# Kernel tuning notes

Hardware: AMD Instinct MI355X
Metric: run time of the kernel (lower is better)

The kernel has to match this reference:

```python
import jax, jax.numpy as jnp
import numpy as np

B, T, C = 2, 2048, 2048
NUM_HEADS, NUM_KV_HEADS, HEAD_DIM = 16, 4, 128
ROPE_THETA = 10000.0
SOFTCAP = 50.0


def sine_table(features, length, min_timescale=1.0, max_timescale=10000.0):
    fraction = jnp.arange(0, features, 2, dtype=jnp.float32) / features
    timescale = min_timescale * (max_timescale / min_timescale) ** fraction
    sinusoid = jnp.arange(length, dtype=jnp.float32)[:, None] / timescale[None, :]
    sinusoid = jnp.concatenate([sinusoid, sinusoid], axis=-1)
    return jnp.sin(sinusoid), jnp.cos(sinusoid)


def rotate_half(x):
    x1, x2 = jnp.split(x, 2, axis=-1)
    return jnp.concatenate([-x2, x1], axis=-1)


def setup_inputs() -> dict:
    key = jax.random.key(0)
    k1, k2, k3, k4, k5 = jax.random.split(key, 5)
    x = jax.random.normal(k1, (B, T, C), dtype=jnp.float32)
    mask = jnp.tril(jnp.ones((T, T), dtype=bool))[None, None]  # causal [1,1,T,T]
    mask = jnp.broadcast_to(mask, (B, 1, T, T))
    std = 0.02
    q_kernel = std * jax.random.normal(k2, (C, NUM_HEADS * HEAD_DIM), dtype=jnp.float32)
    k_kernel = std * jax.random.normal(k3, (C, NUM_KV_HEADS * HEAD_DIM), dtype=jnp.float32)
    v_kernel = std * jax.random.normal(k4, (C, NUM_KV_HEADS * HEAD_DIM), dtype=jnp.float32)
    out_kernel = std * jax.random.normal(k5, (NUM_HEADS * HEAD_DIM, C), dtype=jnp.float32)
    return {"x": x, "mask": mask, "q_kernel": q_kernel, "k_kernel": k_kernel,
            "v_kernel": v_kernel, "out_kernel": out_kernel}


def reference(x, mask, q_kernel, k_kernel, v_kernel, out_kernel):
    _, t, c = x.shape
    r = NUM_HEADS // NUM_KV_HEADS  # GQA group size
    qp = q_kernel.reshape(c, r, NUM_KV_HEADS, HEAD_DIM)
    kp = k_kernel.reshape(c, NUM_KV_HEADS, HEAD_DIM)
    vp = v_kernel.reshape(c, NUM_KV_HEADS, HEAD_DIM)
    op = out_kernel.reshape(r, NUM_KV_HEADS, HEAD_DIM, c)
    q = jnp.einsum('bsm,mrhk->brhsk', x, qp)   # [B,r,h,T,hd]
    k = jnp.einsum('bdm,mhk->bhdk', x, kp)     # [B,h,T,hd]
    v = jnp.einsum('bdm,mhv->bhdv', x, vp)     # [B,h,T,hd]
    sin, cos = sine_table(HEAD_DIM, t, max_timescale=ROPE_THETA)  # [T,hd]
    q = q * cos + rotate_half(q) * sin  # broadcast over leading dims (time at -2)
    k = k * cos + rotate_half(k) * sin
    scale = jax.lax.rsqrt(jnp.array(HEAD_DIM, dtype=x.dtype))
    qk = jnp.einsum('brhsk,bhdk->brhsd', q, k) * scale  # [B,r,h,T,T]
    qk = jnp.tanh(qk / SOFTCAP) * SOFTCAP  # logit softcap
    m = jnp.expand_dims(mask, axis=1)  # [B,1,1,T,T]
    qk = jax.nn.softmax(qk.astype(jnp.float32), where=m).astype(x.dtype)
    qkv = jnp.einsum('brhsd,bhdv->brhsv', qk, v)
    out = jnp.einsum('brhsv,rhvm->bsm', qkv, op)
    return out
```

## Files before the change

### kernel.cpp

```cpp
#include <hip/hip_runtime.h>
#include <hip/hip_bf16.h>

typedef __hip_bfloat16 bf16;
typedef __attribute__((ext_vector_type(8))) short bf16x8;
typedef __attribute__((ext_vector_type(4))) short bf16x4;
typedef __attribute__((ext_vector_type(4))) float f32x4;

#define BATCH 2
#define SEQ 2048
#define CDIM 2048
#define NH 16
#define NKV 4
#define HD 128
#define NQKV 3072

__device__ __forceinline__ float tof(float x)  { return x; }
__device__ __forceinline__ float tof(bf16 x)   { return __bfloat162float(x); }
__device__ __forceinline__ void  stf(float* p, float v) { *p = v; }
__device__ __forceinline__ void  stf(bf16* p,  float v) { *p = __float2bfloat16(v); }

__device__ __forceinline__ void gl_lds16(const bf16* g, bf16* l) {
    typedef const __attribute__((address_space(1))) unsigned int* gp_t;
    typedef __attribute__((address_space(3))) unsigned int* lp_t;
    __builtin_amdgcn_global_load_lds((gp_t)g, (lp_t)l, 16, 0, 0);
}

__device__ __forceinline__ f32x4 mfma16x16x16_bf16(bf16x4 a, bf16x4 b, f32x4 c) {
#if __has_builtin(__builtin_amdgcn_mfma_f32_16x16x16bf16_1k)
    return __builtin_amdgcn_mfma_f32_16x16x16bf16_1k(a, b, c, 0, 0, 0);
#else
    asm volatile("v_mfma_f32_16x16x16_bf16 %0, %1, %2, %0"
                 : "+v"(c) : "v"(a), "v"(b));
    return c;
#endif
}

__device__ __forceinline__ float fast_exp2(float x) {
#if __has_builtin(__builtin_amdgcn_exp2f)
    return __builtin_amdgcn_exp2f(x);
#else
    return exp2f(x);
#endif
}

__global__ __launch_bounds__(256) void f2b_kernel(const float* __restrict__ in,
                                                  bf16* __restrict__ out, int n4)
{
    int i = blockIdx.x * 256 + threadIdx.x;
    if (i >= n4) return;
    float4 v = *(const float4*)&in[(size_t)i * 4];
    bf16 o[4] = {__float2bfloat16(v.x), __float2bfloat16(v.y),
                 __float2bfloat16(v.z), __float2bfloat16(v.w)};
    *(ushort4*)&out[(size_t)i * 4] = *(ushort4*)o;
}

__global__ __launch_bounds__(256) void transpose_f2b_kernel(
    const float* __restrict__ in, bf16* __restrict__ out, int R, int Cn)
{
    __shared__ float tile[64][65];
    const int r0 = blockIdx.y * 64, c0 = blockIdx.x * 64;
    for (int f = threadIdx.x; f < 4096; f += 256) {
        int r = f >> 6, c = f & 63;
        tile[r][c] = in[(size_t)(r0 + r) * Cn + c0 + c];
    }
    __syncthreads();
    for (int f = threadIdx.x; f < 4096; f += 256) {
        int r = f >> 6, c = f & 63;
        out[(size_t)(c0 + r) * R + r0 + c] = __float2bfloat16(tile[c][r]);
    }
}

__global__ __launch_bounds__(256) void vtrans_kernel(
    const bf16* __restrict__ in, bf16* __restrict__ out)
{
    __shared__ bf16 tile[64][65];
    const int b = blockIdx.z;
    const int t0 = blockIdx.y * 64, c0 = blockIdx.x * 64;
    for (int f = threadIdx.x; f < 4096; f += 256) {
        int r = f >> 6, c = f & 63;
        tile[r][c] = in[(size_t)(b * SEQ + t0 + r) * (NKV * HD) + c0 + c];
    }
    __syncthreads();
    for (int f = threadIdx.x; f < 4096; f += 256) {
        int r = f >> 6, c = f & 63;
        out[(size_t)(b * NKV * HD + c0 + r) * SEQ + t0 + c] = tile[c][r];
    }
}

__global__ __launch_bounds__(256) void gemm_qkv_kernel(
    const bf16* __restrict__ A, const bf16* __restrict__ Bt,
    bf16* __restrict__ Qr, bf16* __restrict__ Kr, bf16* __restrict__ Vr,
    int M, int K)
{
    __shared__ __align__(16) bf16 As[128 * 32];
    __shared__ __align__(16) bf16 Bs[128 * 32];

    const int tid = threadIdx.x;
    const int lane = tid & 63;
    const int wave = tid >> 6;
    const int m0 = blockIdx.y * 128;
    const int n0 = blockIdx.x * 128;
    const int wm = (wave >> 1) * 64;
    const int wn = (wave & 1) * 64;
    const int quad = lane >> 4;
    const int l16 = lane & 15;

    const int srow = tid >> 2;
    const int scol = (tid & 3) * 8;
    const bf16* Ag0 = A  + (size_t)(m0 + srow) * K + scol;
    const bf16* Ag1 = A  + (size_t)(m0 + srow + 64) * K + scol;
    const bf16* Bg0 = Bt + (size_t)(n0 + srow) * K + scol;
    const bf16* Bg1 = Bt + (size_t)(n0 + srow + 64) * K + scol;

    f32x4 acc[4][4];
#pragma unroll
    for (int mi = 0; mi < 4; ++mi)
#pragma unroll
        for (int ni = 0; ni < 4; ++ni)
            acc[mi][ni] = (f32x4){0.f, 0.f, 0.f, 0.f};

    for (int kt = 0; kt < K; kt += 32) {
        __syncthreads();
        gl_lds16(Ag0 + kt, &As[tid * 8]);
        gl_lds16(Ag1 + kt, &As[2048 + tid * 8]);
        gl_lds16(Bg0 + kt, &Bs[tid * 8]);
        gl_lds16(Bg1 + kt, &Bs[2048 + tid * 8]);
        __syncthreads();

        bf16x8 a[4], b[4];
#pragma unroll
        for (int mi = 0; mi < 4; ++mi)
            a[mi] = *(const bf16x8*)&As[(wm + mi * 16 + l16) * 32 + quad * 8];
#pragma unroll
        for (int ni = 0; ni < 4; ++ni)
            b[ni] = *(const bf16x8*)&Bs[(wn + ni * 16 + l16) * 32 + quad * 8];
#pragma unroll
        for (int mi = 0; mi < 4; ++mi)
#pragma unroll
            for (int ni = 0; ni < 4; ++ni)
                acc[mi][ni] = __builtin_amdgcn_mfma_f32_16x16x32_bf16(
                    a[mi], b[ni], acc[mi][ni], 0, 0, 0);
    }

    bf16* Cp; int Nst, cbase;
    if (n0 < 2048)      { Cp = Qr; Nst = 2048; cbase = n0; }
    else if (n0 < 2560) { Cp = Kr; Nst = 512;  cbase = n0 - 2048; }
    else                { Cp = Vr; Nst = 512;  cbase = n0 - 2560; }

#pragma unroll
    for (int mi = 0; mi < 4; ++mi)
#pragma unroll
        for (int ni = 0; ni < 4; ++ni) {
            int col = cbase + wn + ni * 16 + l16;
#pragma unroll
            for (int r = 0; r < 4; ++r) {
                int row = m0 + wm + mi * 16 + quad * 4 + r;
                Cp[(size_t)row * Nst + col] = __float2bfloat16(acc[mi][ni][r]);
            }
        }
}

template <typename TC>
__global__ __launch_bounds__(256) void gemm_mfma_bt(
    const bf16* __restrict__ A, const bf16* __restrict__ Bt, TC* __restrict__ C,
    int M, int N, int K)
{
    __shared__ __align__(16) bf16 As[128 * 32];
    __shared__ __align__(16) bf16 Bs[128 * 32];

    const int tid = threadIdx.x;
    const int lane = tid & 63;
    const int wave = tid >> 6;
    const int m0 = blockIdx.y * 128;
    const int n0 = blockIdx.x * 128;
    const int wm = (wave >> 1) * 64;
    const int wn = (wave & 1) * 64;
    const int quad = lane >> 4;
    const int l16 = lane & 15;

    const int srow = tid >> 2;
    const int scol = (tid & 3) * 8;
    const bf16* Ag0 = A  + (size_t)(m0 + srow) * K + scol;
    const bf16* Ag1 = A  + (size_t)(m0 + srow + 64) * K + scol;
    const bf16* Bg0 = Bt + (size_t)(n0 + srow) * K + scol;
    const bf16* Bg1 = Bt + (size_t)(n0 + srow + 64) * K + scol;

    f32x4 acc[4][4];
#pragma unroll
    for (int mi = 0; mi < 4; ++mi)
#pragma unroll
        for (int ni = 0; ni < 4; ++ni)
            acc[mi][ni] = (f32x4){0.f, 0.f, 0.f, 0.f};

    for (int kt = 0; kt < K; kt += 32) {
        __syncthreads();
        gl_lds16(Ag0 + kt, &As[tid * 8]);
        gl_lds16(Ag1 + kt, &As[2048 + tid * 8]);
        gl_lds16(Bg0 + kt, &Bs[tid * 8]);
        gl_lds16(Bg1 + kt, &Bs[2048 + tid * 8]);
        __syncthreads();

        bf16x8 a[4], b[4];
#pragma unroll
        for (int mi = 0; mi < 4; ++mi)
            a[mi] = *(const bf16x8*)&As[(wm + mi * 16 + l16) * 32 + quad * 8];
#pragma unroll
        for (int ni = 0; ni < 4; ++ni)
            b[ni] = *(const bf16x8*)&Bs[(wn + ni * 16 + l16) * 32 + quad * 8];
#pragma unroll
        for (int mi = 0; mi < 4; ++mi)
#pragma unroll
            for (int ni = 0; ni < 4; ++ni)
                acc[mi][ni] = __builtin_amdgcn_mfma_f32_16x16x32_bf16(
                    a[mi], b[ni], acc[mi][ni], 0, 0, 0);
    }

#pragma unroll
    for (int mi = 0; mi < 4; ++mi)
#pragma unroll
        for (int ni = 0; ni < 4; ++ni) {
            int col = n0 + wn + ni * 16 + l16;
#pragma unroll
            for (int r = 0; r < 4; ++r) {
                int row = m0 + wm + mi * 16 + quad * 4 + r;
                stf(&C[(size_t)row * N + col], acc[mi][ni][r]);
            }
        }
}

__global__ __launch_bounds__(256) void rope_kernel(bf16* __restrict__ data,
                                                   int ncols, int total_pairs)
{
    int idx = blockIdx.x * 256 + threadIdx.x;
    if (idx >= total_pairs) return;
    int half = ncols >> 1;
    int row = idx / half;
    int p = idx - row * half;
    int head = p >> 6;
    int i = p & 63;
    int t = row & (SEQ - 1);
    float inv_ts = expf(-(float)i * 0.14391156831212787f);
    float angle = (float)t * inv_ts;
    float s, c;
    sincosf(angle, &s, &c);
    size_t base = (size_t)row * ncols + head * 128 + i;
    float x1 = __bfloat162float(data[base]);
    float x2 = __bfloat162float(data[base + 64]);
    data[base]      = __float2bfloat16(x1 * c - x2 * s);
    data[base + 64] = __float2bfloat16(x2 * c + x1 * s);
}

__global__ __launch_bounds__(256, 3) void attn_mfma4_kernel(
    const bf16* __restrict__ Q, const bf16* __restrict__ K,
    const bf16* __restrict__ Vt, bf16* __restrict__ Att)
{
    __shared__ __align__(16) char smem[34816];
    bf16* Ks  = (bf16*)smem;
    bf16* Vts = (bf16*)(smem + 16384);
    float* CB = (float*)smem;
    __shared__ float lbuf[2][2][16];

    const int tid = threadIdx.x;
    const int lane = tid & 63;
    const int w = tid >> 6;
    const int kw = w >> 1;
    const int qw = w & 1;
    const int quad = lane >> 4;
    const int l16 = lane & 15;
    const int bh = blockIdx.y;
    const int b = bh >> 4;
    const int hq = bh & 15;
    const int kvh = hq & 3;
    const int qt = (gridDim.x - 1) - blockIdx.x;
    const int q0 = qt * 64 + qw * 32;

    bf16x8 qf[2][4];
#pragma unroll
    for (int g = 0; g < 2; ++g) {
        size_t qrow = (size_t)(b * SEQ + q0 + g * 16 + l16) * (NH * HD) + hq * HD;
#pragma unroll
        for (int kk = 0; kk < 4; ++kk)
            qf[g][kk] = *(const bf16x8*)&Q[qrow + kk * 32 + quad * 8];
    }

    const bf16* Kb = K  + (size_t)(b * SEQ) * (NKV * HD) + kvh * HD;
    const bf16* Vb = Vt + (size_t)((b * NKV + kvh) * HD) * SEQ;

    f32x4 O[2][8];
#pragma unroll
    for (int g = 0; g < 2; ++g)
#pragma unroll
        for (int dj = 0; dj < 8; ++dj) O[g][dj] = (f32x4){0.f, 0.f, 0.f, 0.f};
    float lsum[2] = {0.f, 0.f};

    const int srowK = tid >> 4;
    const int sgcK  = (tid & 15) ^ srowK;
    const int srowV = tid >> 3;
    const int sgcV  = (tid & 7) ^ (srowV & 7);

    const int ntiles = qt + 1;
    for (int jt = 0; jt < ntiles; ++jt) {
        const int j0 = jt * 64;
        __syncthreads();
#pragma unroll
        for (int c = 0; c < 4; ++c) {
            gl_lds16(Kb + (size_t)(j0 + c * 16 + srowK) * (NKV * HD) + sgcK * 8,
                     Ks + c * 2048 + tid * 8);
            gl_lds16(Vb + (size_t)(c * 32 + srowV) * SEQ + j0 + sgcV * 8,
                     Vts + c * 2048 + tid * 8);
        }
        __syncthreads();

        f32x4 sacc[2][2];
#pragma unroll
        for (int mt = 0; mt < 2; ++mt) {
#pragma unroll
            for (int g = 0; g < 2; ++g) sacc[mt][g] = (f32x4){0.f, 0.f, 0.f, 0.f};
            const int krow = (kw * 32 + mt * 16 + l16) * 128;
#pragma unroll
            for (int kk = 0; kk < 4; ++kk) {
                bf16x8 kf = *(const bf16x8*)&Ks[krow + (((kk * 4 + quad) ^ l16) * 8)];
#pragma unroll
                for (int g = 0; g < 2; ++g)
                    sacc[mt][g] = __builtin_amdgcn_mfma_f32_16x16x32_bf16(
                        kf, qf[g][kk], sacc[mt][g], 0, 0, 0);
            }
        }

        const bool diag = (jt == qt);
        bf16x4 pf[2][2];
#pragma unroll
        for (int mt = 0; mt < 2; ++mt)
#pragma unroll
            for (int g = 0; g < 2; ++g) {
                bf16 pb[4];
#pragma unroll
                for (int r = 0; r < 4; ++r) {
                    float u = sacc[mt][g][r];
                    float t2 = u * u;
                    float num = fmaf(t2, 9.96274e-4f, 8607.814f);
                    float den = fmaf(t2, 0.0703125f, 67500.f);
                    float s2 = u * num * __builtin_amdgcn_rcpf(den);
                    float p = fast_exp2(s2);
                    if (diag) {
                        int kl = kw * 32 + mt * 16 + quad * 4 + r;
                        int ql = qw * 32 + g * 16 + l16;
                        p = (kl <= ql) ? p : 0.f;
                    }
                    lsum[g] += p;
                    pb[r] = __float2bfloat16(p);
                }
                pf[mt][g] = *(bf16x4*)pb;
            }

#pragma unroll
        for (int dj = 0; dj < 8; ++dj) {
            const int vrow = (dj * 16 + l16) * 64;
            const int dl7 = l16 & 7;
#pragma unroll
            for (int mt = 0; mt < 2; ++mt) {
                int c16 = kw * 4 + mt * 2 + (quad >> 1);
                bf16x4 vf = *(const bf16x4*)&Vts[vrow + ((c16 ^ dl7) << 3)
                                                 + (quad & 1) * 4];
#pragma unroll
                for (int g = 0; g < 2; ++g)
                    O[g][dj] = mfma16x16x16_bf16(vf, pf[mt][g], O[g][dj]);
            }
        }
    }

    float lg[2];
#pragma unroll
    for (int g = 0; g < 2; ++g) {
        float v = lsum[g];
        v += __shfl_xor(v, 16);
        v += __shfl_xor(v, 32);
        lg[g] = v;
    }
    __syncthreads();
    if (kw == 0) {
#pragma unroll
        for (int g = 0; g < 2; ++g) {
#pragma unroll
            for (int dj = 0; dj < 8; ++dj) {
                int basei = ((qw * 2 + g) * 8 + dj) * 272;
#pragma unroll
                for (int r = 0; r < 4; ++r)
                    CB[basei + (quad * 4 + r) * 17 + l16] = O[g][dj][r];
            }
            if (quad == 0) lbuf[qw][g][l16] = lg[g];
        }
    }
    __syncthreads();
    if (kw == 1) {
#pragma unroll
        for (int g = 0; g < 2; ++g) {
            float inv = 1.f / (lg[g] + lbuf[qw][g][l16]);
            size_t obase = (size_t)(b * SEQ + q0 + g * 16 + l16) * (NH * HD) + hq * HD;
#pragma unroll
            for (int dj = 0; dj < 8; ++dj) {
                int basei = ((qw * 2 + g) * 8 + dj) * 272;
                bf16 ob[4];
#pragma unroll
                for (int r = 0; r < 4; ++r) {
                    float v = O[g][dj][r] + CB[basei + (quad * 4 + r) * 17 + l16];
                    ob[r] = __float2bfloat16(v * inv);
                }
                *(ushort4*)&Att[obase + dj * 16 + quad * 4] = *(ushort4*)ob;
            }
        }
    }
}

extern "C" void kernel_launch(void* const* d_in, const int* in_sizes, int n_in,
                              void* d_out, int out_size, void* d_ws, size_t ws_size,
                              hipStream_t stream) {
    const float* x        = (const float*)d_in[0];
    const float* q_kernel = (const float*)d_in[2];
    const float* k_kernel = (const float*)d_in[3];
    const float* v_kernel = (const float*)d_in[4];
    const float* o_kernel = (const float*)d_in[5];
    float* out = (float*)d_out;

    const int M = BATCH * SEQ;
    char* ws = (char*)d_ws;
    bf16* xb   = (bf16*)ws;
    bf16* Att  = xb;
    bf16* wT   = (bf16*)(ws + 16777216);
    bf16* wTq  = wT;
    bf16* wTk  = wT + (size_t)2048 * 2048;
    bf16* wTv  = wT + (size_t)2560 * 2048;
    bf16* woT  = wT;
    bf16* Vt_g = (bf16*)(ws + 25165824);
    bf16* Qr   = (bf16*)(ws + 29360128);
    bf16* Kr   = (bf16*)(ws + 46137344);
    bf16* Vr   = (bf16*)(ws + 50331648);

    f2b_kernel<<<(M * CDIM / 4 + 255) / 256, 256, 0, stream>>>(x, xb, M * CDIM / 4);
    transpose_f2b_kernel<<<dim3((NH * HD) / 64, CDIM / 64), 256, 0, stream>>>(
        q_kernel, wTq, CDIM, NH * HD);
    transpose_f2b_kernel<<<dim3((NKV * HD) / 64, CDIM / 64), 256, 0, stream>>>(
        k_kernel, wTk, CDIM, NKV * HD);
    transpose_f2b_kernel<<<dim3((NKV * HD) / 64, CDIM / 64), 256, 0, stream>>>(
        v_kernel, wTv, CDIM, NKV * HD);

    gemm_qkv_kernel<<<dim3(NQKV / 128, M / 128), 256, 0, stream>>>(
        xb, wT, Qr, Kr, Vr, M, CDIM);

    transpose_f2b_kernel<<<dim3(CDIM / 64, CDIM / 64), 256, 0, stream>>>(
        o_kernel, woT, CDIM, CDIM);

    {
        int pairs_q = M * (NH * HD / 2);
        rope_kernel<<<pairs_q / 256, 256, 0, stream>>>(Qr, NH * HD, pairs_q);
        int pairs_k = M * (NKV * HD / 2);
        rope_kernel<<<pairs_k / 256, 256, 0, stream>>>(Kr, NKV * HD, pairs_k);
    }

    vtrans_kernel<<<dim3((NKV * HD) / 64, SEQ / 64, BATCH), 256, 0, stream>>>(Vr, Vt_g);

    attn_mfma4_kernel<<<dim3(SEQ / 64, BATCH * NH), 256, 0, stream>>>(
        Qr, Kr, Vt_g, Att);

    gemm_mfma_bt<float><<<dim3(CDIM / 128, M / 128), 256, 0, stream>>>(
        Att, woT, out, M, CDIM, CDIM);
}
```

Before: 422.5 us.

## Share K/V tiles across two GQA query heads per block instead of splitting keys

The attention block now handles two query heads that share the same KV head, one per warp pair, and each warp walks the full 64-key tile in two halves. Before, the warp pairs split the keys of a single head. Each K/V tile loaded into shared memory is therefore reused by two heads, and the grid shrinks from B*16 to B*8 rows. The cross-warp reduction of partial O and row sums through shared memory and its extra syncs are removed. In exchange there are half as many blocks and each warp does twice the per-tile work, which could lower parallelism on a large-CU GPU.

```diff
diff --git a/kernel.cpp b/kernel.cpp
--- a/kernel.cpp
+++ b/kernel.cpp
@@ -250,27 +250,26 @@
     data[base + 64] = __float2bfloat16(x2 * c + x1 * s);
 }
 
-__global__ __launch_bounds__(256, 3) void attn_mfma4_kernel(
+__global__ __launch_bounds__(256, 3) void attn_mfma5_kernel(
     const bf16* __restrict__ Q, const bf16* __restrict__ K,
     const bf16* __restrict__ Vt, bf16* __restrict__ Att)
 {
-    __shared__ __align__(16) char smem[34816];
+    __shared__ __align__(16) char smem[32768];
     bf16* Ks  = (bf16*)smem;
     bf16* Vts = (bf16*)(smem + 16384);
-    float* CB = (float*)smem;
-    __shared__ float lbuf[2][2][16];
 
     const int tid = threadIdx.x;
     const int lane = tid & 63;
     const int w = tid >> 6;
-    const int kw = w >> 1;
+    const int hs = w >> 1;
     const int qw = w & 1;
     const int quad = lane >> 4;
     const int l16 = lane & 15;
     const int bh = blockIdx.y;
-    const int b = bh >> 4;
-    const int hq = bh & 15;
-    const int kvh = hq & 3;
+    const int b   = bh >> 3;
+    const int kvh = (bh >> 1) & 3;
+    const int pr  = bh & 1;
+    const int hq  = kvh + 4 * (pr * 2 + hs);
     const int qt = (gridDim.x - 1) - blockIdx.x;
     const int q0 = qt * 64 + qw * 32;
 
@@ -311,103 +310,81 @@
         }
         __syncthreads();
 
-        f32x4 sacc[2][2];
-#pragma unroll
-        for (int mt = 0; mt < 2; ++mt) {
-#pragma unroll
-            for (int g = 0; g < 2; ++g) sacc[mt][g] = (f32x4){0.f, 0.f, 0.f, 0.f};
-            const int krow = (kw * 32 + mt * 16 + l16) * 128;
-#pragma unroll
-            for (int kk = 0; kk < 4; ++kk) {
-                bf16x8 kf = *(const bf16x8*)&Ks[krow + (((kk * 4 + quad) ^ l16) * 8)];
-#pragma unroll
-                for (int g = 0; g < 2; ++g)
-                    sacc[mt][g] = __builtin_amdgcn_mfma_f32_16x16x32_bf16(
-                        kf, qf[g][kk], sacc[mt][g], 0, 0, 0);
+        const bool diag = (jt == qt);
+#pragma unroll
+        for (int half = 0; half < 2; ++half) {
+            f32x4 sacc[2][2];
+#pragma unroll
+            for (int mt = 0; mt < 2; ++mt) {
+#pragma unroll
+                for (int g = 0; g < 2; ++g) sacc[mt][g] = (f32x4){0.f, 0.f, 0.f, 0.f};
+                const int krow = (half * 32 + mt * 16 + l16) * 128;
+#pragma unroll
+                for (int kk = 0; kk < 4; ++kk) {
+                    bf16x8 kf = *(const bf16x8*)&Ks[krow + (((kk * 4 + quad) ^ l16) * 8)];
+#pragma unroll
+                    for (int g = 0; g < 2; ++g)
+                        sacc[mt][g] = __builtin_amdgcn_mfma_f32_16x16x32_bf16(
+                            kf, qf[g][kk], sacc[mt][g], 0, 0, 0);
+                }
+            }
+
+            bf16x4 pf[2][2];
+#pragma unroll
+            for (int mt = 0; mt < 2; ++mt)
+#pragma unroll
+                for (int g = 0; g < 2; ++g) {
+                    bf16 pb[4];
+#pragma unroll
+                    for (int r = 0; r < 4; ++r) {
+                        float u = sacc[mt][g][r];
+                        float t2 = u * u;
+                        float num = fmaf(t2, 9.96274e-4f, 8607.814f);
+                        float den = fmaf(t2, 0.0703125f, 67500.f);
+                        float s2 = u * num * __builtin_amdgcn_rcpf(den);
+                        float p = fast_exp2(s2);
+                        if (diag) {
+                            int kl = half * 32 + mt * 16 + quad * 4 + r;
+                            int ql = qw * 32 + g * 16 + l16;
+                            p = (kl <= ql) ? p : 0.f;
+                        }
+                        lsum[g] += p;
+                        pb[r] = __float2bfloat16(p);
+                    }
+                    pf[mt][g] = *(bf16x4*)pb;
+                }
+
+#pragma unroll
+            for (int dj = 0; dj < 8; ++dj) {
+                const int vrow = (dj * 16 + l16) * 64;
+                const int dl7 = l16 & 7;
+#pragma unroll
+                for (int mt = 0; mt < 2; ++mt) {
+                    int c16 = half * 4 + mt * 2 + (quad >> 1);
+                    bf16x4 vf = *(const bf16x4*)&Vts[vrow + ((c16 ^ dl7) << 3)
+                                                     + (quad & 1) * 4];
+#pragma unroll
+                    for (int g = 0; g < 2; ++g)
+                        O[g][dj] = mfma16x16x16_bf16(vf, pf[mt][g], O[g][dj]);
+                }
             }
         }
-
-        const bool diag = (jt == qt);
-        bf16x4 pf[2][2];
-#pragma unroll
-        for (int mt = 0; mt < 2; ++mt)
-#pragma unroll
-            for (int g = 0; g < 2; ++g) {
-                bf16 pb[4];
-#pragma unroll
-                for (int r = 0; r < 4; ++r) {
-                    float u = sacc[mt][g][r];
-                    float t2 = u * u;
-                    float num = fmaf(t2, 9.96274e-4f, 8607.814f);
-                    float den = fmaf(t2, 0.0703125f, 67500.f);
-                    float s2 = u * num * __builtin_amdgcn_rcpf(den);
-                    float p = fast_exp2(s2);
-                    if (diag) {
-                        int kl = kw * 32 + mt * 16 + quad * 4 + r;
-                        int ql = qw * 32 + g * 16 + l16;
-                        p = (kl <= ql) ? p : 0.f;
-                    }
-                    lsum[g] += p;
-                    pb[r] = __float2bfloat16(p);
-                }
-                pf[mt][g] = *(bf16x4*)pb;
-            }
-
-#pragma unroll
-        for (int dj = 0; dj < 8; ++dj) {
-            const int vrow = (dj * 16 + l16) * 64;
-            const int dl7 = l16 & 7;
-#pragma unroll
-            for (int mt = 0; mt < 2; ++mt) {
-                int c16 = kw * 4 + mt * 2 + (quad >> 1);
-                bf16x4 vf = *(const bf16x4*)&Vts[vrow + ((c16 ^ dl7) << 3)
-                                                 + (quad & 1) * 4];
-#pragma unroll
-                for (int g = 0; g < 2; ++g)
-                    O[g][dj] = mfma16x16x16_bf16(vf, pf[mt][g], O[g][dj]);
-            }
-        }
-    }
-
-    float lg[2];
+    }
+
 #pragma unroll
     for (int g = 0; g < 2; ++g) {
         float v = lsum[g];
         v += __shfl_xor(v, 16);
         v += __shfl_xor(v, 32);
-        lg[g] = v;
-    }
-    __syncthreads();
-    if (kw == 0) {
-#pragma unroll
-        for (int g = 0; g < 2; ++g) {
-#pragma unroll
-            for (int dj = 0; dj < 8; ++dj) {
-                int basei = ((qw * 2 + g) * 8 + dj) * 272;
-#pragma unroll
-                for (int r = 0; r < 4; ++r)
-                    CB[basei + (quad * 4 + r) * 17 + l16] = O[g][dj][r];
-            }
-            if (quad == 0) lbuf[qw][g][l16] = lg[g];
-        }
-    }
-    __syncthreads();
-    if (kw == 1) {
-#pragma unroll
-        for (int g = 0; g < 2; ++g) {
-            float inv = 1.f / (lg[g] + lbuf[qw][g][l16]);
-            size_t obase = (size_t)(b * SEQ + q0 + g * 16 + l16) * (NH * HD) + hq * HD;
-#pragma unroll
-            for (int dj = 0; dj < 8; ++dj) {
-                int basei = ((qw * 2 + g) * 8 + dj) * 272;
-                bf16 ob[4];
-#pragma unroll
-                for (int r = 0; r < 4; ++r) {
-                    float v = O[g][dj][r] + CB[basei + (quad * 4 + r) * 17 + l16];
-                    ob[r] = __float2bfloat16(v * inv);
-                }
-                *(ushort4*)&Att[obase + dj * 16 + quad * 4] = *(ushort4*)ob;
-            }
+        float inv = 1.f / v;
+        size_t obase = (size_t)(b * SEQ + q0 + g * 16 + l16) * (NH * HD) + hq * HD;
+#pragma unroll
+        for (int dj = 0; dj < 8; ++dj) {
+            bf16 ob[4];
+#pragma unroll
+            for (int r = 0; r < 4; ++r)
+                ob[r] = __float2bfloat16(O[g][dj][r] * inv);
+            *(ushort4*)&Att[obase + dj * 16 + quad * 4] = *(ushort4*)ob;
         }
     }
 }
@@ -459,7 +436,7 @@
 
     vtrans_kernel<<<dim3((NKV * HD) / 64, SEQ / 64, BATCH), 256, 0, stream>>>(Vr, Vt_g);
 
-    attn_mfma4_kernel<<<dim3(SEQ / 64, BATCH * NH), 256, 0, stream>>>(
+    attn_mfma5_kernel<<<dim3(SEQ / 64, BATCH * NKV * 2), 256, 0, stream>>>(
         Qr, Kr, Vt_g, Att);
 
     gemm_mfma_bt<float><<<dim3(CDIM / 128, M / 128), 256, 0, stream>>>(
```

New measurement: 400.7 us. -5.2%, faster.
